# Kernel optimization log

Hardware: AMD Instinct MI355X
Metric: run time of the kernel (lower is better)

The kernel has to match this reference:

```python
import jax, jax.numpy as jnp
import numpy as np

N0, N1, N2 = 320000, 80000, 16000
E1, E2 = 800000, 160000
IN_C, HID, OUT_C = 128, 64, 48
H1, H2 = 4, 1
NEG_SLOPE = 0.2  # PyG GATv2Conv default leaky_relu slope


def _glorot(key, shape):
    fan_in = shape[0]
    return jax.random.normal(key, shape, jnp.float32) / jnp.sqrt(jnp.asarray(fan_in, jnp.float32))


def setup_inputs() -> dict:
    key = jax.random.key(0)
    ks = jax.random.split(key, 12)
    inp = {
        "x": jax.random.normal(ks[0], (N0, IN_C), jnp.float32),
        # layer 1: GATv2Conv(IN_C -> HID, heads=H1, concat=True)
        "Wl1": _glorot(ks[1], (IN_C, H1 * HID)),
        "bl1": jnp.zeros((H1 * HID,), jnp.float32),
        "Wr1": _glorot(ks[2], (IN_C, H1 * HID)),
        "br1": jnp.zeros((H1 * HID,), jnp.float32),
        "att1": jax.random.normal(ks[3], (H1, HID), jnp.float32) * 0.1,
        "bias1": jnp.zeros((H1 * HID,), jnp.float32),
        # layer 2: GATv2Conv(H1*HID -> OUT_C, heads=H2, concat=False)
        "Wl2": _glorot(ks[4], (H1 * HID, H2 * OUT_C)),
        "bl2": jnp.zeros((H2 * OUT_C,), jnp.float32),
        "Wr2": _glorot(ks[5], (H1 * HID, H2 * OUT_C)),
        "br2": jnp.zeros((H2 * OUT_C,), jnp.float32),
        "att2": jax.random.normal(ks[6], (H2, OUT_C), jnp.float32) * 0.1,
        "bias2": jnp.zeros((OUT_C,), jnp.float32),
        # sampled bipartite edge lists (edge j->i: src index into x_src, dst into x_dst)
        "src1": jax.random.randint(ks[7], (E1,), 0, N0, jnp.int32),
        "dst1": jax.random.randint(ks[8], (E1,), 0, N1, jnp.int32),
        "src2": jax.random.randint(ks[9], (E2,), 0, N1, jnp.int32),
        "dst2": jax.random.randint(ks[10], (E2,), 0, N2, jnp.int32),
        "n1": N1,
        "n2": N2,
    }
    return inp


def gatv2_conv(x_src, x_dst, src, dst, Wl, bl, Wr, br, att, bias, n_dst, concat):
    H, C = att.shape
    xl = (x_src @ Wl + bl).reshape(-1, H, C)   # [N_src, H, C] (source transform)
    xr = (x_dst @ Wr + br).reshape(-1, H, C)   # [N_dst, H, C] (target transform)
    e = xl[src] + xr[dst]                      # [E, H, C]
    e = jnp.where(e > 0, e, NEG_SLOPE * e)     # leaky_relu (GATv2: nonlinearity before att)
    alpha = jnp.einsum('ehc,hc->eh', e, att)   # [E, H] attention logits
    # softmax over edges sharing the same target node
    amax = jax.ops.segment_max(alpha, dst, num_segments=n_dst)
    ex = jnp.exp(alpha - amax[dst])
    denom = jax.ops.segment_sum(ex, dst, num_segments=n_dst)
    w = ex / (denom[dst] + 1e-16)              # [E, H]
    out = jax.ops.segment_sum(xl[src] * w[:, :, None], dst, num_segments=n_dst)  # [N_dst, H, C]
    out = out.reshape(n_dst, H * C) if concat else out.mean(axis=1)
    return out + bias


def reference(x, Wl1, bl1, Wr1, br1, att1, bias1, Wl2, bl2, Wr2, br2, att2, bias2,
              src1, dst1, src2, dst2, n1, n2):
    h = gatv2_conv(x, x[:n1], src1, dst1, Wl1, bl1, Wr1, br1, att1, bias1, n1, True)
    h = jax.nn.relu(h)
    # dropout is identity in eval mode
    h = gatv2_conv(h, h[:n2], src2, dst2, Wl2, bl2, Wr2, br2, att2, bias2, n2, False)
    return jax.nn.log_softmax(h, axis=-1)
```

## Files before the change

kernel.cpp:

```cpp
#include <hip/hip_runtime.h>
#include <hip/hip_bf16.h>

#define N0_  320000
#define N1_  80000
#define N2_  16000
#define INC_ 128
#define HID_ 64
#define H1_  4
#define C1_  256
#define OUT_ 48
#define OUTP_ 64
#define NEG_ 0.2f

typedef __attribute__((ext_vector_type(8))) short bfrag8;
typedef __attribute__((ext_vector_type(4))) float ffrag4;

__device__ __forceinline__ float bf2f(unsigned short u){
  unsigned int v = ((unsigned int)u) << 16;
  return __uint_as_float(v);
}
__device__ __forceinline__ unsigned short f2bf(float f){
  unsigned int u = __float_as_uint(f);
  u += 0x7FFFu + ((u >> 16) & 1u);
  return (unsigned short)(u >> 16);
}
__device__ __forceinline__ void unpack2(unsigned int u, float& lo, float& hi){
  lo = __uint_as_float(u << 16);
  hi = __uint_as_float(u & 0xffff0000u);
}

__global__ void transpose_to_bf16(const float* __restrict__ W,
                                  unsigned short* __restrict__ Wt, int K, int N){
  int idx = blockIdx.x*256 + threadIdx.x;
  if (idx >= K*N) return;
  int n = idx / K, k = idx - n*K;
  Wt[idx] = f2bf(W[(size_t)k*N + n]);
}

__global__ __launch_bounds__(256, 3) void gemm_mfma_k128n256(
    const float* __restrict__ X, const unsigned short* __restrict__ Wt,
    const float* __restrict__ bias, unsigned short* __restrict__ out)
{
  __shared__ unsigned short As[64][136];
  __shared__ unsigned short Cs[64][264];
  const int t = threadIdx.x;
  const int lane = t & 63, wave = t >> 6;
  const int row0 = blockIdx.x << 6;
  const int l15 = lane & 15, q = lane >> 4;
  const int wcol = wave << 6;

  bfrag8 bfr[4][4];
  #pragma unroll
  for (int nt = 0; nt < 4; ++nt)
    #pragma unroll
    for (int ks = 0; ks < 4; ++ks)
      bfr[nt][ks] = *(const bfrag8*)(Wt + (size_t)(wcol + (nt<<4) + l15)*128 + (ks<<5) + (q<<3));

  const int c4 = t & 31;
  #pragma unroll
  for (int i = 0; i < 8; ++i){
    int r = (i<<3) + (t>>5);
    float4 xv = *(const float4*)(X + ((size_t)(row0 + r) << 7) + (c4<<2));
    ushort4 s; s.x=f2bf(xv.x); s.y=f2bf(xv.y); s.z=f2bf(xv.z); s.w=f2bf(xv.w);
    *(ushort4*)(&As[r][c4<<2]) = s;
  }
  __syncthreads();

  ffrag4 z = {0.f, 0.f, 0.f, 0.f};
  ffrag4 acc[4][4];
  #pragma unroll
  for (int mt = 0; mt < 4; ++mt)
    #pragma unroll
    for (int nt = 0; nt < 4; ++nt) acc[mt][nt] = z;

  #pragma unroll
  for (int mt = 0; mt < 4; ++mt){
    #pragma unroll
    for (int ks = 0; ks < 4; ++ks){
      bfrag8 af = *(const bfrag8*)(&As[(mt<<4) + l15][(ks<<5) + (q<<3)]);
      #pragma unroll
      for (int nt = 0; nt < 4; ++nt)
        acc[mt][nt] = __builtin_amdgcn_mfma_f32_16x16x32_bf16(af, bfr[nt][ks], acc[mt][nt], 0, 0, 0);
    }
  }

  float bb[4];
  #pragma unroll
  for (int nt = 0; nt < 4; ++nt) bb[nt] = bias[wcol + (nt<<4) + l15];
  #pragma unroll
  for (int mt = 0; mt < 4; ++mt)
    #pragma unroll
    for (int nt = 0; nt < 4; ++nt)
      #pragma unroll
      for (int rg = 0; rg < 4; ++rg)
        Cs[(mt<<4) + (q<<2) + rg][wcol + (nt<<4) + l15] = f2bf(acc[mt][nt][rg] + bb[nt]);
  __syncthreads();
  #pragma unroll
  for (int i = 0; i < 8; ++i){
    int r = (i<<3) + (t>>5);
    *(bfrag8*)(out + ((size_t)(row0 + r) << 8) + (c4<<3)) = *(const bfrag8*)(&Cs[r][c4<<3]);
  }
}

__global__ __launch_bounds__(256) void gemm_mfma_k256n48(
    const unsigned short* __restrict__ Hin, const unsigned short* __restrict__ Wt,
    const float* __restrict__ bias, float* __restrict__ out)
{
  __shared__ unsigned short As2[64][264];
  __shared__ unsigned short Bs2[48][264];
  const int t = threadIdx.x;
  const int lane = t & 63, wave = t >> 6;
  const int row0 = blockIdx.x << 6;
  const int l15 = lane & 15, q = lane >> 4;

  const int c32 = t & 31;
  #pragma unroll
  for (int i = 0; i < 8; ++i){
    int r = (i<<3) + (t>>5);
    *(bfrag8*)(&As2[r][c32<<3]) = *(const bfrag8*)(Hin + ((size_t)(row0 + r) << 8) + (c32<<3));
  }
  #pragma unroll
  for (int i = 0; i < 6; ++i){
    int idx = i*256 + t;
    int r = idx >> 5, c = (idx & 31) << 3;
    *(bfrag8*)(&Bs2[r][c]) = *(const bfrag8*)(Wt + (size_t)r*256 + c);
  }
  __syncthreads();

  ffrag4 z = {0.f, 0.f, 0.f, 0.f};
  ffrag4 acc[3] = {z, z, z};
  #pragma unroll
  for (int ks = 0; ks < 8; ++ks){
    bfrag8 af = *(const bfrag8*)(&As2[(wave<<4) + l15][(ks<<5) + (q<<3)]);
    #pragma unroll
    for (int nt = 0; nt < 3; ++nt){
      bfrag8 bf = *(const bfrag8*)(&Bs2[(nt<<4) + l15][(ks<<5) + (q<<3)]);
      acc[nt] = __builtin_amdgcn_mfma_f32_16x16x32_bf16(af, bf, acc[nt], 0, 0, 0);
    }
  }
  #pragma unroll
  for (int nt = 0; nt < 3; ++nt){
    int col = (nt<<4) + l15;
    float bb = bias[col];
    #pragma unroll
    for (int rg = 0; rg < 4; ++rg){
      int row = row0 + (wave<<4) + (q<<2) + rg;
      out[(size_t)row*OUTP_ + col] = acc[nt][rg] + bb;
    }
  }
  #pragma unroll
  for (int rg = 0; rg < 4; ++rg){
    int row = row0 + (wave<<4) + (q<<2) + rg;
    out[(size_t)row*OUTP_ + 48 + l15] = 0.f;
  }
}

__global__ void hist_k(const int* __restrict__ dst, int* __restrict__ counts, int E){
  int i = blockIdx.x*blockDim.x + threadIdx.x;
  if (i < E) atomicAdd(&counts[dst[i]], 1);
}

__global__ __launch_bounds__(256) void scan_local(const int* __restrict__ in,
    int* __restrict__ excl, int* __restrict__ partials, int n){
  __shared__ int s[256];
  int t = threadIdx.x, i = blockIdx.x*256 + t;
  int v = (i < n) ? in[i] : 0;
  s[t] = v; __syncthreads();
  #pragma unroll
  for (int off = 1; off < 256; off <<= 1){
    int u = (t >= off) ? s[t-off] : 0;
    __syncthreads();
    s[t] += u; __syncthreads();
  }
  if (i < n) excl[i] = s[t] - v;
  if (t == 255) partials[blockIdx.x] = s[255];
}

__global__ __launch_bounds__(512) void scan_partials(int* __restrict__ partials, int nb){
  __shared__ int s[512];
  int t = threadIdx.x;
  int v = (t < nb) ? partials[t] : 0;
  s[t] = v; __syncthreads();
  #pragma unroll
  for (int off = 1; off < 512; off <<= 1){
    int u = (t >= off) ? s[t-off] : 0;
    __syncthreads();
    s[t] += u; __syncthreads();
  }
  if (t < nb) partials[t] = s[t] - v;
}

__global__ void scan_finalize(int* __restrict__ excl, const int* __restrict__ partials,
    int* __restrict__ cursor, int n){
  int i = blockIdx.x*256 + threadIdx.x;
  if (i >= n) return;
  int o = excl[i] + partials[blockIdx.x];
  excl[i] = o; cursor[i] = o;
}

__global__ void scatter_k(const int* __restrict__ src, const int* __restrict__ dst,
    int* __restrict__ cursor, int* __restrict__ perm, int E){
  int i = blockIdx.x*blockDim.x + threadIdx.x;
  if (i >= E) return;
  int pos = atomicAdd(&cursor[dst[i]], 1);
  perm[pos] = src[i];
}

__global__ __launch_bounds__(256) void gat_aggregate1(
    const unsigned short* __restrict__ xl, const unsigned short* __restrict__ xr,
    const int* __restrict__ offsets, const int* __restrict__ counts,
    const int* __restrict__ perm, const float* __restrict__ att,
    const float* __restrict__ bias, unsigned short* __restrict__ hout, int n)
{
  int node = (blockIdx.x << 2) + (threadIdx.x >> 6);
  if (node >= n) return;
  const int lane = threadIdx.x & 63;
  const int slot = lane >> 5;
  const int sub  = lane & 31;
  const int elem = sub << 3;
  const unsigned int ebyte = (unsigned)elem << 1;
  const char* xlb = (const char*)xl;

  uint4 ru = *(const uint4*)(xr + ((size_t)node << 8) + elem);
  float r[8];
  unpack2(ru.x, r[0], r[1]); unpack2(ru.y, r[2], r[3]);
  unpack2(ru.z, r[4], r[5]); unpack2(ru.w, r[6], r[7]);
  float4 al = *(const float4*)(att + elem);
  float4 ah = *(const float4*)(att + elem + 4);
  float a[8] = {al.x, al.y, al.z, al.w, ah.x, ah.y, ah.z, ah.w};

  float acc[8] = {0,0,0,0,0,0,0,0};
  float den = 0.f;
  const int st = offsets[node], cnt = counts[node];

  for (int jb = 0; jb < cnt; jb += 64){
    int m = cnt - jb; if (m > 64) m = 64;
    int pv = (lane < m) ? perm[st + jb + lane] : 0;
    #pragma unroll 2
    for (int j = 0; j < m; j += 2){
      int idx = j + slot;
      int s = __shfl(pv, idx);
      uint4 xu = *(const uint4*)(xlb + (((unsigned)s << 9) + ebyte));
      float x[8];
      unpack2(xu.x, x[0], x[1]); unpack2(xu.y, x[2], x[3]);
      unpack2(xu.z, x[4], x[5]); unpack2(xu.w, x[6], x[7]);
      float p = 0.f;
      #pragma unroll
      for (int i = 0; i < 8; ++i){
        float v = x[i] + r[i];
        float e = fmaf(NEG_, fminf(v, 0.f), fmaxf(v, 0.f));
        p = fmaf(e, a[i], p);
      }
      p += __shfl_xor(p, 1);
      p += __shfl_xor(p, 2);
      p += __shfl_xor(p, 4);
      float ex = __expf(p);
      ex = (idx < m) ? ex : 0.f;
      den += ex;
      #pragma unroll
      for (int i = 0; i < 8; ++i) acc[i] = fmaf(ex, x[i], acc[i]);
    }
  }
  den += __shfl_xor(den, 32);
  #pragma unroll
  for (int i = 0; i < 8; ++i) acc[i] += __shfl_xor(acc[i], 32);

  if (slot == 0){
    float w = 1.f / (den + 1e-16f);
    float4 bl = *(const float4*)(bias + elem);
    float4 bh = *(const float4*)(bias + elem + 4);
    float b[8] = {bl.x, bl.y, bl.z, bl.w, bh.x, bh.y, bh.z, bh.w};
    unsigned int o[4];
    #pragma unroll
    for (int i = 0; i < 4; ++i){
      unsigned short lo = f2bf(fmaxf(fmaf(acc[2*i],   w, b[2*i]),   0.f));
      unsigned short hi = f2bf(fmaxf(fmaf(acc[2*i+1], w, b[2*i+1]), 0.f));
      o[i] = (unsigned)lo | ((unsigned)hi << 16);
    }
    *(uint4*)(hout + ((size_t)node << 8) + elem) = make_uint4(o[0], o[1], o[2], o[3]);
  }
}

__global__ __launch_bounds__(256) void gat_aggregate2(
    const float* __restrict__ xl, const float* __restrict__ xr,
    const int* __restrict__ offsets, const int* __restrict__ counts,
    const int* __restrict__ perm, const float* __restrict__ att,
    const float* __restrict__ bias, float* __restrict__ out, int n)
{
  int node = (blockIdx.x << 2) + (threadIdx.x >> 6);
  if (node >= n) return;
  const int lane = threadIdx.x & 63;
  const int slot = lane >> 4;
  const int sub  = lane & 15;
  const bool realc = sub < 12;

  float4 r = *(const float4*)(xr + (size_t)node*OUTP_ + (sub<<2));
  float4 a = realc ? *(const float4*)(att + (sub<<2)) : make_float4(0,0,0,0);
  float4 acc = make_float4(0,0,0,0);
  float den = 0.f;
  const int st = offsets[node], cnt = counts[node];

  for (int jb = 0; jb < cnt; jb += 64){
    int m = cnt - jb; if (m > 64) m = 64;
    int pv = (lane < m) ? perm[st + jb + lane] : 0;
    #pragma unroll 2
    for (int j = 0; j < m; j += 4){
      int idx = j + slot;
      int s = __shfl(pv, idx);
      float4 xv = *(const float4*)(xl + (size_t)((unsigned)s*OUTP_ + (sub<<2)));
      float v0 = xv.x + r.x, v1 = xv.y + r.y, v2 = xv.z + r.z, v3 = xv.w + r.w;
      float p;
      p = fmaf(a.x, fmaf(NEG_, fminf(v0,0.f), fmaxf(v0,0.f)), 0.f);
      p = fmaf(a.y, fmaf(NEG_, fminf(v1,0.f), fmaxf(v1,0.f)), p);
      p = fmaf(a.z, fmaf(NEG_, fminf(v2,0.f), fmaxf(v2,0.f)), p);
      p = fmaf(a.w, fmaf(NEG_, fminf(v3,0.f), fmaxf(v3,0.f)), p);
      p += __shfl_xor(p, 1);
      p += __shfl_xor(p, 2);
      p += __shfl_xor(p, 4);
      p += __shfl_xor(p, 8);
      float ex = __expf(p);
      ex = (idx < m) ? ex : 0.f;
      den += ex;
      acc.x = fmaf(ex, xv.x, acc.x); acc.y = fmaf(ex, xv.y, acc.y);
      acc.z = fmaf(ex, xv.z, acc.z); acc.w = fmaf(ex, xv.w, acc.w);
    }
  }
  den += __shfl_xor(den, 16); den += __shfl_xor(den, 32);
  acc.x += __shfl_xor(acc.x, 16); acc.x += __shfl_xor(acc.x, 32);
  acc.y += __shfl_xor(acc.y, 16); acc.y += __shfl_xor(acc.y, 32);
  acc.z += __shfl_xor(acc.z, 16); acc.z += __shfl_xor(acc.z, 32);
  acc.w += __shfl_xor(acc.w, 16); acc.w += __shfl_xor(acc.w, 32);

  float w = 1.f / (den + 1e-16f);
  float4 b = realc ? *(const float4*)(bias + (sub<<2)) : make_float4(0,0,0,0);
  float v0 = fmaf(acc.x, w, b.x), v1 = fmaf(acc.y, w, b.y);
  float v2 = fmaf(acc.z, w, b.z), v3 = fmaf(acc.w, w, b.w);

  float mx = realc ? fmaxf(fmaxf(v0, v1), fmaxf(v2, v3)) : -3.0e38f;
  mx = fmaxf(mx, __shfl_xor(mx, 1)); mx = fmaxf(mx, __shfl_xor(mx, 2));
  mx = fmaxf(mx, __shfl_xor(mx, 4)); mx = fmaxf(mx, __shfl_xor(mx, 8));
  float es = realc ? (__expf(v0-mx) + __expf(v1-mx) + __expf(v2-mx) + __expf(v3-mx)) : 0.f;
  es += __shfl_xor(es, 1); es += __shfl_xor(es, 2);
  es += __shfl_xor(es, 4); es += __shfl_xor(es, 8);
  float ls = __logf(es);
  if (slot == 0 && realc){
    float4 o = make_float4(v0-mx-ls, v1-mx-ls, v2-mx-ls, v3-mx-ls);
    *(float4*)(out + (size_t)node*OUT_ + (sub<<2)) = o;
  }
}

extern "C" void kernel_launch(void* const* d_in, const int* in_sizes, int n_in,
                              void* d_out, int out_size, void* d_ws, size_t ws_size,
                              hipStream_t stream)
{
  const float* x    = (const float*)d_in[0];
  const float* Wl1  = (const float*)d_in[1];
  const float* bl1  = (const float*)d_in[2];
  const float* Wr1  = (const float*)d_in[3];
  const float* br1  = (const float*)d_in[4];
  const float* att1 = (const float*)d_in[5];
  const float* bias1= (const float*)d_in[6];
  const float* Wl2  = (const float*)d_in[7];
  const float* bl2  = (const float*)d_in[8];
  const float* Wr2  = (const float*)d_in[9];
  const float* br2  = (const float*)d_in[10];
  const float* att2 = (const float*)d_in[11];
  const float* bias2= (const float*)d_in[12];
  const int* src1 = (const int*)d_in[13];
  const int* dst1 = (const int*)d_in[14];
  const int* src2 = (const int*)d_in[15];
  const int* dst2 = (const int*)d_in[16];
  const int E1 = in_sizes[13];
  const int E2 = in_sizes[15];
  (void)n_in; (void)out_size; (void)ws_size;

  char* ws = (char*)d_ws;
  unsigned short* xl1  = (unsigned short*)(ws + 0LL);
  unsigned short* xr1  = (unsigned short*)(ws + 163840000LL);
  unsigned short* hbuf = (unsigned short*)(ws + 204800000LL);
  float* xl2p   = (float*)(ws + 245760000LL);
  float* xr2p   = (float*)(ws + 266240000LL);
  int*   perm1  = (int*)  (ws + 270336000LL);
  int*   perm2  = (int*)  (ws + 273536000LL);
  int*   cnt1   = (int*)  (ws + 274176000LL);
  int*   cnt2   = (int*)  (ws + 274496000LL);
  int*   off1   = (int*)  (ws + 274560000LL);
  int*   cur1   = (int*)  (ws + 274880000LL);
  int*   off2   = (int*)  (ws + 275200000LL);
  int*   cur2   = (int*)  (ws + 275264000LL);
  int*   part1  = (int*)  (ws + 275328000LL);
  int*   part2  = (int*)  (ws + 275330048LL);
  unsigned short* Wt1l = (unsigned short*)(ws + 275332096LL);
  unsigned short* Wt1r = (unsigned short*)(ws + 275397632LL);
  unsigned short* Wt2l = (unsigned short*)(ws + 275463168LL);
  unsigned short* Wt2r = (unsigned short*)(ws + 275487744LL);

  hipMemsetAsync(ws + 274176000LL, 0, 384000LL, stream);

  const int nb1 = (N1_ + 255) / 256;
  const int nb2 = (N2_ + 255) / 256;

  transpose_to_bf16<<<128, 256, 0, stream>>>(Wl1, Wt1l, INC_, C1_);
  transpose_to_bf16<<<128, 256, 0, stream>>>(Wr1, Wt1r, INC_, C1_);
  transpose_to_bf16<<< 48, 256, 0, stream>>>(Wl2, Wt2l, C1_, OUT_);
  transpose_to_bf16<<< 48, 256, 0, stream>>>(Wr2, Wt2r, C1_, OUT_);

  gemm_mfma_k128n256<<<N0_/64, 256, 0, stream>>>(x, Wt1l, bl1, xl1);
  gemm_mfma_k128n256<<<N1_/64, 256, 0, stream>>>(x, Wt1r, br1, xr1);

  hist_k       <<<(E1+255)/256, 256, 0, stream>>>(dst1, cnt1, E1);
  scan_local   <<<nb1, 256, 0, stream>>>(cnt1, off1, part1, N1_);
  scan_partials<<<1, 512, 0, stream>>>(part1, nb1);
  scan_finalize<<<nb1, 256, 0, stream>>>(off1, part1, cur1, N1_);
  scatter_k    <<<(E1+255)/256, 256, 0, stream>>>(src1, dst1, cur1, perm1, E1);

  gat_aggregate1<<<(N1_+3)/4, 256, 0, stream>>>(xl1, xr1, off1, cnt1, perm1,
                                                att1, bias1, hbuf, N1_);

  gemm_mfma_k256n48<<<N1_/64, 256, 0, stream>>>(hbuf, Wt2l, bl2, xl2p);
  gemm_mfma_k256n48<<<N2_/64, 256, 0, stream>>>(hbuf, Wt2r, br2, xr2p);

  hist_k       <<<(E2+255)/256, 256, 0, stream>>>(dst2, cnt2, E2);
  scan_local   <<<nb2, 256, 0, stream>>>(cnt2, off2, part2, N2_);
  scan_partials<<<1, 512, 0, stream>>>(part2, nb2);
  scan_finalize<<<nb2, 256, 0, stream>>>(off2, part2, cur2, N2_);
  scatter_k    <<<(E2+255)/256, 256, 0, stream>>>(src2, dst2, cur2, perm2, E2);

  gat_aggregate2<<<(N2_+3)/4, 256, 0, stream>>>(xl2p, xr2p, off2, cnt2, perm2,
                                                att2, bias2, (float*)d_out, N2_);
}
```

Measured before the change: 552.3 us.

## Merge launches for weight transpose, CSR build, and L/R GEMMs; prefetch gathers

```diff
diff --git a/kernel.cpp b/kernel.cpp
--- a/kernel.cpp
+++ b/kernel.cpp
@@ -29,17 +29,22 @@
   hi = __uint_as_float(u & 0xffff0000u);
 }
 
-__global__ void transpose_to_bf16(const float* __restrict__ W,
-                                  unsigned short* __restrict__ Wt, int K, int N){
+__global__ void transpose_all(const float* __restrict__ Wl1, const float* __restrict__ Wr1,
+                              const float* __restrict__ Wl2, const float* __restrict__ Wr2,
+                              unsigned short* __restrict__ Wt1l, unsigned short* __restrict__ Wt1r,
+                              unsigned short* __restrict__ Wt2l, unsigned short* __restrict__ Wt2r){
   int idx = blockIdx.x*256 + threadIdx.x;
-  if (idx >= K*N) return;
-  int n = idx / K, k = idx - n*K;
-  Wt[idx] = f2bf(W[(size_t)k*N + n]);
-}
-
-__global__ __launch_bounds__(256, 3) void gemm_mfma_k128n256(
-    const float* __restrict__ X, const unsigned short* __restrict__ Wt,
-    const float* __restrict__ bias, unsigned short* __restrict__ out)
+  if (idx < 32768){ int n = idx >> 7, k = idx & 127; Wt1l[idx] = f2bf(Wl1[k*C1_ + n]); }
+  else if (idx < 65536){ int j = idx - 32768; int n = j >> 7, k = j & 127; Wt1r[j] = f2bf(Wr1[k*C1_ + n]); }
+  else if (idx < 77824){ int j = idx - 65536; int n = j >> 8, k = j & 255; Wt2l[j] = f2bf(Wl2[k*OUT_ + n]); }
+  else if (idx < 90112){ int j = idx - 77824; int n = j >> 8, k = j & 255; Wt2r[j] = f2bf(Wr2[k*OUT_ + n]); }
+}
+
+__global__ __launch_bounds__(256, 3) void gemm1_fused(
+    const float* __restrict__ X,
+    const unsigned short* __restrict__ Wtl, const unsigned short* __restrict__ Wtr,
+    const float* __restrict__ bl, const float* __restrict__ br,
+    unsigned short* __restrict__ outl, unsigned short* __restrict__ outr)
 {
   __shared__ unsigned short As[64][136];
   __shared__ unsigned short Cs[64][264];
@@ -48,15 +53,8 @@
   const int row0 = blockIdx.x << 6;
   const int l15 = lane & 15, q = lane >> 4;
   const int wcol = wave << 6;
-
-  bfrag8 bfr[4][4];
-  #pragma unroll
-  for (int nt = 0; nt < 4; ++nt)
-    #pragma unroll
-    for (int ks = 0; ks < 4; ++ks)
-      bfr[nt][ks] = *(const bfrag8*)(Wt + (size_t)(wcol + (nt<<4) + l15)*128 + (ks<<5) + (q<<3));
-
   const int c4 = t & 31;
+
   #pragma unroll
   for (int i = 0; i < 8; ++i){
     int r = (i<<3) + (t>>5);
@@ -66,45 +64,62 @@
   }
   __syncthreads();
 
-  ffrag4 z = {0.f, 0.f, 0.f, 0.f};
-  ffrag4 acc[4][4];
-  #pragma unroll
-  for (int mt = 0; mt < 4; ++mt)
-    #pragma unroll
-    for (int nt = 0; nt < 4; ++nt) acc[mt][nt] = z;
-
-  #pragma unroll
-  for (int mt = 0; mt < 4; ++mt){
-    #pragma unroll
-    for (int ks = 0; ks < 4; ++ks){
-      bfrag8 af = *(const bfrag8*)(&As[(mt<<4) + l15][(ks<<5) + (q<<3)]);
+  const int npass = (row0 < N1_) ? 2 : 1;
+  for (int pass = 0; pass < npass; ++pass){
+    const unsigned short* Wt = pass ? Wtr : Wtl;
+    const float* bias = pass ? br : bl;
+    unsigned short* out = pass ? outr : outl;
+
+    bfrag8 bfr[4][4];
+    #pragma unroll
+    for (int nt = 0; nt < 4; ++nt)
+      #pragma unroll
+      for (int ks = 0; ks < 4; ++ks)
+        bfr[nt][ks] = *(const bfrag8*)(Wt + (size_t)(wcol + (nt<<4) + l15)*128 + (ks<<5) + (q<<3));
+
+    ffrag4 z = {0.f, 0.f, 0.f, 0.f};
+    ffrag4 acc[4][4];
+    #pragma unroll
+    for (int mt = 0; mt < 4; ++mt)
+      #pragma unroll
+      for (int nt = 0; nt < 4; ++nt) acc[mt][nt] = z;
+
+    #pragma unroll
+    for (int mt = 0; mt < 4; ++mt){
+      #pragma unroll
+      for (int ks = 0; ks < 4; ++ks){
+        bfrag8 af = *(const bfrag8*)(&As[(mt<<4) + l15][(ks<<5) + (q<<3)]);
+        #pragma unroll
+        for (int nt = 0; nt < 4; ++nt)
+          acc[mt][nt] = __builtin_amdgcn_mfma_f32_16x16x32_bf16(af, bfr[nt][ks], acc[mt][nt], 0, 0, 0);
+      }
+    }
+
+    float bb[4];
+    #pragma unroll
+    for (int nt = 0; nt < 4; ++nt) bb[nt] = bias[wcol + (nt<<4) + l15];
+    #pragma unroll
+    for (int mt = 0; mt < 4; ++mt)
       #pragma unroll
       for (int nt = 0; nt < 4; ++nt)
-        acc[mt][nt] = __builtin_amdgcn_mfma_f32_16x16x32_bf16(af, bfr[nt][ks], acc[mt][nt], 0, 0, 0);
-    }
-  }
-
-  float bb[4];
-  #pragma unroll
-  for (int nt = 0; nt < 4; ++nt) bb[nt] = bias[wcol + (nt<<4) + l15];
-  #pragma unroll
-  for (int mt = 0; mt < 4; ++mt)
-    #pragma unroll
-    for (int nt = 0; nt < 4; ++nt)
-      #pragma unroll
-      for (int rg = 0; rg < 4; ++rg)
-        Cs[(mt<<4) + (q<<2) + rg][wcol + (nt<<4) + l15] = f2bf(acc[mt][nt][rg] + bb[nt]);
-  __syncthreads();
-  #pragma unroll
-  for (int i = 0; i < 8; ++i){
-    int r = (i<<3) + (t>>5);
-    *(bfrag8*)(out + ((size_t)(row0 + r) << 8) + (c4<<3)) = *(const bfrag8*)(&Cs[r][c4<<3]);
-  }
-}
-
-__global__ __launch_bounds__(256) void gemm_mfma_k256n48(
-    const unsigned short* __restrict__ Hin, const unsigned short* __restrict__ Wt,
-    const float* __restrict__ bias, float* __restrict__ out)
+        #pragma unroll
+        for (int rg = 0; rg < 4; ++rg)
+          Cs[(mt<<4) + (q<<2) + rg][wcol + (nt<<4) + l15] = f2bf(acc[mt][nt][rg] + bb[nt]);
+    __syncthreads();
+    #pragma unroll
+    for (int i = 0; i < 8; ++i){
+      int r = (i<<3) + (t>>5);
+      *(bfrag8*)(out + ((size_t)(row0 + r) << 8) + (c4<<3)) = *(const bfrag8*)(&Cs[r][c4<<3]);
+    }
+    if (pass + 1 < npass) __syncthreads();
+  }
+}
+
+__global__ __launch_bounds__(256) void gemm2_fused(
+    const unsigned short* __restrict__ Hin,
+    const unsigned short* __restrict__ Wtl, const unsigned short* __restrict__ Wtr,
+    const float* __restrict__ bl, const float* __restrict__ br,
+    float* __restrict__ outl, float* __restrict__ outr)
 {
   __shared__ unsigned short As2[64][264];
   __shared__ unsigned short Bs2[48][264];
@@ -112,58 +127,74 @@
   const int lane = t & 63, wave = t >> 6;
   const int row0 = blockIdx.x << 6;
   const int l15 = lane & 15, q = lane >> 4;
-
   const int c32 = t & 31;
+
   #pragma unroll
   for (int i = 0; i < 8; ++i){
     int r = (i<<3) + (t>>5);
     *(bfrag8*)(&As2[r][c32<<3]) = *(const bfrag8*)(Hin + ((size_t)(row0 + r) << 8) + (c32<<3));
   }
-  #pragma unroll
-  for (int i = 0; i < 6; ++i){
-    int idx = i*256 + t;
-    int r = idx >> 5, c = (idx & 31) << 3;
-    *(bfrag8*)(&Bs2[r][c]) = *(const bfrag8*)(Wt + (size_t)r*256 + c);
-  }
-  __syncthreads();
-
-  ffrag4 z = {0.f, 0.f, 0.f, 0.f};
-  ffrag4 acc[3] = {z, z, z};
-  #pragma unroll
-  for (int ks = 0; ks < 8; ++ks){
-    bfrag8 af = *(const bfrag8*)(&As2[(wave<<4) + l15][(ks<<5) + (q<<3)]);
+
+  const int npass = (row0 < N2_) ? 2 : 1;
+  for (int pass = 0; pass < npass; ++pass){
+    const unsigned short* Wt = pass ? Wtr : Wtl;
+    const float* bias = pass ? br : bl;
+    float* out = pass ? outr : outl;
+
+    if (pass) __syncthreads();
+    #pragma unroll
+    for (int i = 0; i < 6; ++i){
+      int idx = i*256 + t;
+      int r = idx >> 5, c = (idx & 31) << 3;
+      *(bfrag8*)(&Bs2[r][c]) = *(const bfrag8*)(Wt + (size_t)r*256 + c);
+    }
+    __syncthreads();
+
+    ffrag4 z = {0.f, 0.f, 0.f, 0.f};
+    ffrag4 acc[3] = {z, z, z};
+    #pragma unroll
+    for (int ks = 0; ks < 8; ++ks){
+      bfrag8 af = *(const bfrag8*)(&As2[(wave<<4) + l15][(ks<<5) + (q<<3)]);
+      #pragma unroll
+      for (int nt = 0; nt < 3; ++nt){
+        bfrag8 bf = *(const bfrag8*)(&Bs2[(nt<<4) + l15][(ks<<5) + (q<<3)]);
+        acc[nt] = __builtin_amdgcn_mfma_f32_16x16x32_bf16(af, bf, acc[nt], 0, 0, 0);
+      }
+    }
     #pragma unroll
     for (int nt = 0; nt < 3; ++nt){
-      bfrag8 bf = *(const bfrag8*)(&Bs2[(nt<<4) + l15][(ks<<5) + (q<<3)]);
-      acc[nt] = __builtin_amdgcn_mfma_f32_16x16x32_bf16(af, bf, acc[nt], 0, 0, 0);
-    }
-  }
-  #pragma unroll
-  for (int nt = 0; nt < 3; ++nt){
-    int col = (nt<<4) + l15;
-    float bb = bias[col];
+      int col = (nt<<4) + l15;
+      float bb = bias[col];
+      #pragma unroll
+      for (int rg = 0; rg < 4; ++rg){
+        int row = row0 + (wave<<4) + (q<<2) + rg;
+        out[(size_t)row*OUTP_ + col] = acc[nt][rg] + bb;
+      }
+    }
     #pragma unroll
     for (int rg = 0; rg < 4; ++rg){
       int row = row0 + (wave<<4) + (q<<2) + rg;
-      out[(size_t)row*OUTP_ + col] = acc[nt][rg] + bb;
-    }
-  }
-  #pragma unroll
-  for (int rg = 0; rg < 4; ++rg){
-    int row = row0 + (wave<<4) + (q<<2) + rg;
-    out[(size_t)row*OUTP_ + 48 + l15] = 0.f;
-  }
-}
-
-__global__ void hist_k(const int* __restrict__ dst, int* __restrict__ counts, int E){
-  int i = blockIdx.x*blockDim.x + threadIdx.x;
-  if (i < E) atomicAdd(&counts[dst[i]], 1);
-}
-
-__global__ __launch_bounds__(256) void scan_local(const int* __restrict__ in,
-    int* __restrict__ excl, int* __restrict__ partials, int n){
+      out[(size_t)row*OUTP_ + 48 + l15] = 0.f;
+    }
+  }
+}
+
+__global__ void hist_both(const int* __restrict__ dst1, const int* __restrict__ dst2,
+                          int* __restrict__ cnt1, int* __restrict__ cnt2, int E1, int E2){
+  int i = blockIdx.x*256 + threadIdx.x;
+  if (i < E1) atomicAdd(&cnt1[dst1[i]], 1);
+  else if (i < E1 + E2) atomicAdd(&cnt2[dst2[i - E1]], 1);
+}
+
+__global__ __launch_bounds__(256) void scan_local_both(
+    const int* __restrict__ in1, const int* __restrict__ in2,
+    int* __restrict__ ex1, int* __restrict__ ex2,
+    int* __restrict__ part1, int* __restrict__ part2, int n1, int n2, int nb1){
   __shared__ int s[256];
-  int t = threadIdx.x, i = blockIdx.x*256 + t;
+  const int* in; int* excl; int* partials; int n; int b;
+  if ((int)blockIdx.x < nb1){ in = in1; excl = ex1; partials = part1; n = n1; b = blockIdx.x; }
+  else { in = in2; excl = ex2; partials = part2; n = n2; b = blockIdx.x - nb1; }
+  int t = threadIdx.x, i = b*256 + t;
   int v = (i < n) ? in[i] : 0;
   s[t] = v; __syncthreads();
   #pragma unroll
@@ -173,11 +204,14 @@
     s[t] += u; __syncthreads();
   }
   if (i < n) excl[i] = s[t] - v;
-  if (t == 255) partials[blockIdx.x] = s[255];
-}
-
-__global__ __launch_bounds__(512) void scan_partials(int* __restrict__ partials, int nb){
+  if (t == 255) partials[b] = s[255];
+}
+
+__global__ __launch_bounds__(512) void scan_partials_both(
+    int* __restrict__ part1, int* __restrict__ part2, int nb1, int nb2){
   __shared__ int s[512];
+  int* partials = blockIdx.x ? part2 : part1;
+  int nb = blockIdx.x ? nb2 : nb1;
   int t = threadIdx.x;
   int v = (t < nb) ? partials[t] : 0;
   s[t] = v; __syncthreads();
@@ -190,20 +224,32 @@
   if (t < nb) partials[t] = s[t] - v;
 }
 
-__global__ void scan_finalize(int* __restrict__ excl, const int* __restrict__ partials,
-    int* __restrict__ cursor, int n){
+__global__ void scan_finalize_both(
+    int* __restrict__ ex1, int* __restrict__ ex2,
+    const int* __restrict__ part1, const int* __restrict__ part2,
+    int* __restrict__ cur1, int* __restrict__ cur2, int n1, int n2, int nb1){
+  int* excl; const int* partials; int* cursor; int n; int b;
+  if ((int)blockIdx.x < nb1){ excl = ex1; partials = part1; cursor = cur1; n = n1; b = blockIdx.x; }
+  else { excl = ex2; partials = part2; cursor = cur2; n = n2; b = blockIdx.x - nb1; }
+  int i = b*256 + threadIdx.x;
+  if (i >= n) return;
+  int o = excl[i] + partials[b];
+  excl[i] = o; cursor[i] = o;
+}
+
+__global__ void scatter_both(const int* __restrict__ src1, const int* __restrict__ dst1,
+                             const int* __restrict__ src2, const int* __restrict__ dst2,
+                             int* __restrict__ cur1, int* __restrict__ cur2,
+                             int* __restrict__ perm1, int* __restrict__ perm2, int E1, int E2){
   int i = blockIdx.x*256 + threadIdx.x;
-  if (i >= n) return;
-  int o = excl[i] + partials[blockIdx.x];
-  excl[i] = o; cursor[i] = o;
-}
-
-__global__ void scatter_k(const int* __restrict__ src, const int* __restrict__ dst,
-    int* __restrict__ cursor, int* __restrict__ perm, int E){
-  int i = blockIdx.x*blockDim.x + threadIdx.x;
-  if (i >= E) return;
-  int pos = atomicAdd(&cursor[dst[i]], 1);
-  perm[pos] = src[i];
+  if (i < E1){
+    int pos = atomicAdd(&cur1[dst1[i]], 1);
+    perm1[pos] = src1[i];
+  } else if (i < E1 + E2){
+    int j = i - E1;
+    int pos = atomicAdd(&cur2[dst2[j]], 1);
+    perm2[pos] = src2[j];
+  }
 }
 
 __global__ __launch_bounds__(256) void gat_aggregate1(
@@ -221,6 +267,7 @@
   const unsigned int ebyte = (unsigned)elem << 1;
   const char* xlb = (const char*)xl;
 
+  const int st = offsets[node], cnt = counts[node];
   uint4 ru = *(const uint4*)(xr + ((size_t)node << 8) + elem);
   float r[8];
   unpack2(ru.x, r[0], r[1]); unpack2(ru.y, r[2], r[3]);
@@ -231,19 +278,18 @@
 
   float acc[8] = {0,0,0,0,0,0,0,0};
   float den = 0.f;
-  const int st = offsets[node], cnt = counts[node];
 
   for (int jb = 0; jb < cnt; jb += 64){
     int m = cnt - jb; if (m > 64) m = 64;
     int pv = (lane < m) ? perm[st + jb + lane] : 0;
-    #pragma unroll 2
+    int s_cur = __shfl(pv, slot);
+    uint4 xc = *(const uint4*)(xlb + (((unsigned)s_cur << 9) + ebyte));
     for (int j = 0; j < m; j += 2){
-      int idx = j + slot;
-      int s = __shfl(pv, idx);
-      uint4 xu = *(const uint4*)(xlb + (((unsigned)s << 9) + ebyte));
+      int s_next = __shfl(pv, (j + 2 + slot) & 63);
+      uint4 xn = *(const uint4*)(xlb + (((unsigned)s_next << 9) + ebyte));
       float x[8];
-      unpack2(xu.x, x[0], x[1]); unpack2(xu.y, x[2], x[3]);
-      unpack2(xu.z, x[4], x[5]); unpack2(xu.w, x[6], x[7]);
+      unpack2(xc.x, x[0], x[1]); unpack2(xc.y, x[2], x[3]);
+      unpack2(xc.z, x[4], x[5]); unpack2(xc.w, x[6], x[7]);
       float p = 0.f;
       #pragma unroll
       for (int i = 0; i < 8; ++i){
@@ -255,10 +301,11 @@
       p += __shfl_xor(p, 2);
       p += __shfl_xor(p, 4);
       float ex = __expf(p);
-      ex = (idx < m) ? ex : 0.f;
+      ex = (j + slot < m) ? ex : 0.f;
       den += ex;
       #pragma unroll
       for (int i = 0; i < 8; ++i) acc[i] = fmaf(ex, x[i], acc[i]);
+      xc = xn;
     }
   }
   den += __shfl_xor(den, 32);
@@ -294,21 +341,21 @@
   const int sub  = lane & 15;
   const bool realc = sub < 12;
 
+  const int st = offsets[node], cnt = counts[node];
   float4 r = *(const float4*)(xr + (size_t)node*OUTP_ + (sub<<2));
   float4 a = realc ? *(const float4*)(att + (sub<<2)) : make_float4(0,0,0,0);
   float4 acc = make_float4(0,0,0,0);
   float den = 0.f;
-  const int st = offsets[node], cnt = counts[node];
 
   for (int jb = 0; jb < cnt; jb += 64){
     int m = cnt - jb; if (m > 64) m = 64;
     int pv = (lane < m) ? perm[st + jb + lane] : 0;
-    #pragma unroll 2
+    int s_cur = __shfl(pv, slot);
+    float4 xc = *(const float4*)(xl + (size_t)((unsigned)s_cur*OUTP_ + (sub<<2)));
     for (int j = 0; j < m; j += 4){
-      int idx = j + slot;
-      int s = __shfl(pv, idx);
-      float4 xv = *(const float4*)(xl + (size_t)((unsigned)s*OUTP_ + (sub<<2)));
-      float v0 = xv.x + r.x, v1 = xv.y + r.y, v2 = xv.z + r.z, v3 = xv.w + r.w;
+      int s_next = __shfl(pv, (j + 4 + slot) & 63);
+      float4 xn = *(const float4*)(xl + (size_t)((unsigned)s_next*OUTP_ + (sub<<2)));
+      float v0 = xc.x + r.x, v1 = xc.y + r.y, v2 = xc.z + r.z, v3 = xc.w + r.w;
       float p;
       p = fmaf(a.x, fmaf(NEG_, fminf(v0,0.f), fmaxf(v0,0.f)), 0.f);
       p = fmaf(a.y, fmaf(NEG_, fminf(v1,0.f), fmaxf(v1,0.f)), p);
@@ -319,10 +366,11 @@
       p += __shfl_xor(p, 4);
       p += __shfl_xor(p, 8);
       float ex = __expf(p);
-      ex = (idx < m) ? ex : 0.f;
+      ex = (j + slot < m) ? ex : 0.f;
       den += ex;
-      acc.x = fmaf(ex, xv.x, acc.x); acc.y = fmaf(ex, xv.y, acc.y);
-      acc.z = fmaf(ex, xv.z, acc.z); acc.w = fmaf(ex, xv.w, acc.w);
+      acc.x = fmaf(ex, xc.x, acc.x); acc.y = fmaf(ex, xc.y, acc.y);
+      acc.z = fmaf(ex, xc.z, acc.z); acc.w = fmaf(ex, xc.w, acc.w);
+      xc = xn;
     }
   }
   den += __shfl_xor(den, 16); den += __shfl_xor(den, 32);
@@ -400,31 +448,21 @@
   const int nb1 = (N1_ + 255) / 256;
   const int nb2 = (N2_ + 255) / 256;
 
-  transpose_to_bf16<<<128, 256, 0, stream>>>(Wl1, Wt1l, INC_, C1_);
-  transpose_to_bf16<<<128, 256, 0, stream>>>(Wr1, Wt1r, INC_, C1_);
-  transpose_to_bf16<<< 48, 256, 0, stream>>>(Wl2, Wt2l, C1_, OUT_);
-  transpose_to_bf16<<< 48, 256, 0, stream>>>(Wr2, Wt2r, C1_, OUT_);
-
-  gemm_mfma_k128n256<<<N0_/64, 256, 0, stream>>>(x, Wt1l, bl1, xl1);
-  gemm_mfma_k128n256<<<N1_/64, 256, 0, stream>>>(x, Wt1r, br1, xr1);
-
-  hist_k       <<<(E1+255)/256, 256, 0, stream>>>(dst1, cnt1, E1);
-  scan_local   <<<nb1, 256, 0, stream>>>(cnt1, off1, part1, N1_);
-  scan_partials<<<1, 512, 0, stream>>>(part1, nb1);
-  scan_finalize<<<nb1, 256, 0, stream>>>(off1, part1, cur1, N1_);
-  scatter_k    <<<(E1+255)/256, 256, 0, stream>>>(src1, dst1, cur1, perm1, E1);
+  transpose_all<<<352, 256, 0, stream>>>(Wl1, Wr1, Wl2, Wr2, Wt1l, Wt1r, Wt2l, Wt2r);
+
+  hist_both         <<<(E1+E2+255)/256, 256, 0, stream>>>(dst1, dst2, cnt1, cnt2, E1, E2);
+  scan_local_both   <<<nb1+nb2, 256, 0, stream>>>(cnt1, cnt2, off1, off2, part1, part2, N1_, N2_, nb1);
+  scan_partials_both<<<2, 512, 0, stream>>>(part1, part2, nb1, nb2);
+  scan_finalize_both<<<nb1+nb2, 256, 0, stream>>>(off1, off2, part1, part2, cur1, cur2, N1_, N2_, nb1);
+  scatter_both      <<<(E1+E2+255)/256, 256, 0, stream>>>(src1, dst1, src2, dst2,
+                                                          cur1, cur2, perm1, perm2, E1, E2);
+
+  gemm1_fused<<<N0_/64, 256, 0, stream>>>(x, Wt1l, Wt1r, bl1, br1, xl1, xr1);
 
   gat_aggregate1<<<(N1_+3)/4, 256, 0, stream>>>(xl1, xr1, off1, cnt1, perm1,
                                                 att1, bias1, hbuf, N1_);
 
-  gemm_mfma_k256n48<<<N1_/64, 256, 0, stream>>>(hbuf, Wt2l, bl2, xl2p);
-  gemm_mfma_k256n48<<<N2_/64, 256, 0, stream>>>(hbuf, Wt2r, br2, xr2p);
-
-  hist_k       <<<(E2+255)/256, 256, 0, stream>>>(dst2, cnt2, E2);
-  scan_local   <<<nb2, 256, 0, stream>>>(cnt2, off2, part2, N2_);
-  scan_partials<<<1, 512, 0, stream>>>(part2, nb2);
-  scan_finalize<<<nb2, 256, 0, stream>>>(off2, part2, cur2, N2_);
-  scatter_k    <<<(E2+255)/256, 256, 0, stream>>>(src2, dst2, cur2, perm2, E2);
+  gemm2_fused<<<N1_/64, 256, 0, stream>>>(hbuf, Wt2l, Wt2r, bl2, br2, xl2p, xr2p);
 
   gat_aggregate2<<<(N2_+3)/4, 256, 0, stream>>>(xl2p, xr2p, off2, cnt2, perm2,
                                                 att2, bias2, (float*)d_out, N2_);
```

Result: faster. 535.2 us (-3.1%).
